# Performance work log

Measured on AMD Instinct MI355X. Metric: run time of the kernel, lower is better.

Reference implementation:

```python
import jax, jax.numpy as jnp
import numpy as np

B = 2097152  # flattened batch of 3x3 rotation matrices

def setup_inputs() -> dict:
    key = jax.random.key(0)
    k1, k2 = jax.random.split(key)
    # scale by 0.1 so cos=(trace(m1 m2^T)-1)/2 stays strictly inside (-1,1)
    pred_rot = jax.random.normal(k1, (B, 3, 3), dtype=jnp.float32) * 0.1
    gt_rot = jax.random.normal(k2, (B, 3, 3), dtype=jnp.float32) * 0.1
    return {"pred_rot": pred_rot, "gt_rot": gt_rot}

def reference(pred_rot, gt_rot):
    m1 = pred_rot.reshape(-1, 3, 3)
    m2 = gt_rot.reshape(-1, 3, 3)
    # trace(m1 @ m2^T) == sum(m1 * m2) elementwise -> avoid the bmm
    cos = (jnp.einsum('bij,bij->b', m1, m2) - 1.0) * 0.5
    cos = jnp.clip(cos, -1.0, 1.0)  # min with +1, max with -1
    theta = jnp.arccos(cos)
    return jnp.mean(theta)  # reduction='mean'
```

## Files before the change

### kernel.cpp

```cpp
#include <hip/hip_runtime.h>
#include <math.h>


typedef float f4 __attribute__((ext_vector_type(4)));

#define TPB 256
#define NBLOCKS 2048

#define LOADQ(P, pa, pb)                                                    \
    P##A0 = __builtin_nontemporal_load((pa) + q);                           \
    P##A1 = __builtin_nontemporal_load((pa) + 4 + q);                       \
    P##A2 = __builtin_nontemporal_load((pa) + 8);                           \
    P##B0 = __builtin_nontemporal_load((pb) + q);                           \
    P##B1 = __builtin_nontemporal_load((pb) + 4 + q);                       \
    P##B2 = __builtin_nontemporal_load((pb) + 8);

__global__ __launch_bounds__(TPB) void geo_partial(
    const float* __restrict__ a, const float* __restrict__ b,
    float* __restrict__ ws, float* __restrict__ out, float invM, int M,
    int use_atomic)
{
    __shared__ float wsum[TPB / 64];
    const int tid = threadIdx.x;
    const int q   = tid & 3;

    float sum = 0.0f;

    const long long G    = (long long)M >> 2;
    const long long Q0   = (long long)blockIdx.x * (TPB / 4) + (tid >> 2);
    const long long Qstr = (long long)gridDim.x * (TPB / 4);

    const f4* __restrict__ a4 = (const f4*)a;
    const f4* __restrict__ b4 = (const f4*)b;

    f4 A0, A1, A2, B0, B1, B2;
    long long Q = Q0;
    if (Q < G) {
        const f4* pa = a4 + 9 * Q;
        const f4* pb = b4 + 9 * Q;
        LOADQ(, pa, pb)
    }

    while (Q < G) {
        const long long Qn = Q + Qstr;
        f4 NA0, NA1, NA2, NB0, NB1, NB2;
        if (Qn < G) {
            const f4* pa = a4 + 9 * Qn;
            const f4* pb = b4 + 9 * Qn;
            LOADQ(N, pa, pb)
        }

        f4 t0, t1;
        t0.x = A0.x * B0.x; t0.y = A0.y * B0.y;
        t0.z = A0.z * B0.z; t0.w = A0.w * B0.w;
        t1.x = A1.x * B1.x; t1.y = A1.y * B1.y;
        t1.z = A1.z * B1.z; t1.w = A1.w * B1.w;

        const float c01 = t0.x + t0.y;
        const float T0  = (c01 + t0.z) + t0.w;
        const float d01 = t1.x + t1.y;
        const float T1  = (d01 + t1.z) + t1.w;

        float P0 = (q == 3) ? 0.0f : ((q == 2) ? t0.x : T0);
        float P1 = (q == 0) ? d01  : ((q == 1) ? 0.0f
                   : ((q == 2) ? (T0 - t0.x) : T0));
        float P2 = (q == 0) ? (T1 - d01) : ((q == 1) ? T1
                   : ((q == 2) ? (T1 - t1.w) : 0.0f));
        float P3 = (q == 2) ? t1.w : ((q == 3) ? T1 : 0.0f);

        P0 += __shfl_xor(P0, 1, 64); P0 += __shfl_xor(P0, 2, 64);
        P1 += __shfl_xor(P1, 1, 64); P1 += __shfl_xor(P1, 2, 64);
        P2 += __shfl_xor(P2, 1, 64); P2 += __shfl_xor(P2, 2, 64);
        P3 += __shfl_xor(P3, 1, 64); P3 += __shfl_xor(P3, 2, 64);

        const float u0 = A2.x * B2.x, u1 = A2.y * B2.y;
        const float u2 = A2.z * B2.z, u3 = A2.w * B2.w;
        const float dl2 = (u0 + u1) + (u2 + u3);

        const float d = (q == 0) ? P0 : (q == 1) ? P1
                      : (q == 2) ? P2 : (P3 + dl2);
        const float cv = fminf(1.0f, fmaxf(-1.0f, (d - 1.0f) * 0.5f));
        sum += acosf(cv);

        if (Qn < G) {
            A0 = NA0; A1 = NA1; A2 = NA2;
            B0 = NB0; B1 = NB1; B2 = NB2;
        }
        Q = Qn;
    }

    {
        const long long gid    = (long long)blockIdx.x * TPB + tid;
        const long long stride = (long long)gridDim.x * TPB;
        for (long long m = 4 * G + gid; m < M; m += stride) {
            float dd = 0.0f;
            #pragma unroll
            for (int j = 0; j < 9; ++j)
                dd = fmaf(a[m * 9 + j], b[m * 9 + j], dd);
            sum += acosf(fminf(1.0f, fmaxf(-1.0f, (dd - 1.0f) * 0.5f)));
        }
    }

    #pragma unroll
    for (int off = 32; off > 0; off >>= 1)
        sum += __shfl_down(sum, off, 64);
    if ((tid & 63) == 0) wsum[tid >> 6] = sum;
    __syncthreads();
    if (tid == 0) {
        float s = 0.0f;
        #pragma unroll
        for (int i = 0; i < TPB / 64; ++i) s += wsum[i];
        if (use_atomic) atomicAdd(out, s * invM);
        else            ws[blockIdx.x] = s;
    }
}

__global__ __launch_bounds__(256) void geo_finish(
    const float* __restrict__ ws, float* __restrict__ out,
    float invM, int nb)
{
    __shared__ float wsum[4];
    float s = 0.0f;
    for (int i = threadIdx.x; i < nb; i += 256) s += ws[i];
    #pragma unroll
    for (int off = 32; off > 0; off >>= 1)
        s += __shfl_down(s, off, 64);
    if ((threadIdx.x & 63) == 0) wsum[threadIdx.x >> 6] = s;
    __syncthreads();
    if (threadIdx.x == 0)
        out[0] = (wsum[0] + wsum[1] + wsum[2] + wsum[3]) * invM;
}

extern "C" void kernel_launch(void* const* d_in, const int* in_sizes, int n_in,
                              void* d_out, int out_size, void* d_ws, size_t ws_size,
                              hipStream_t stream) {
    const float* a = (const float*)d_in[0];
    const float* b = (const float*)d_in[1];
    float* out = (float*)d_out;

    const int n = in_sizes[0];
    const int M = n / 9;

    const bool ws_ok = (ws_size >= (size_t)NBLOCKS * sizeof(float));
    if (!ws_ok) {
        hipMemsetAsync(out, 0, (size_t)out_size * sizeof(float), stream);
    }
    geo_partial<<<NBLOCKS, TPB, 0, stream>>>(
        a, b, (float*)d_ws, out, 1.0f / (float)M, M, ws_ok ? 0 : 1);
    if (ws_ok) {
        geo_finish<<<1, 256, 0, stream>>>(
            (const float*)d_ws, out, 1.0f / (float)M, NBLOCKS);
    }
}
```

Baseline: 162.7 us.

## Process 16 matrices per quad with fully coalesced strided f4 loads

Each group of four lanes now handles 16 matrices (144 floats) at a time, issuing 9 interleaved f4 loads per lane so that consecutive lanes read consecutive 16-byte chunks. The old layout had every lane re-read a shared third vector and only partly coalesced its accesses. The manual software prefetch of the next iteration is dropped in favour of 18 independent loads in flight per iteration. The cost is more registers and more select logic per element, plus four shuffle reductions and acos calls per loop iteration.

```diff
diff --git a/kernel.cpp b/kernel.cpp
--- a/kernel.cpp
+++ b/kernel.cpp
@@ -6,14 +6,6 @@
 
 #define TPB 256
 #define NBLOCKS 2048
-
-#define LOADQ(P, pa, pb)                                                    \
-    P##A0 = __builtin_nontemporal_load((pa) + q);                           \
-    P##A1 = __builtin_nontemporal_load((pa) + 4 + q);                       \
-    P##A2 = __builtin_nontemporal_load((pa) + 8);                           \
-    P##B0 = __builtin_nontemporal_load((pb) + q);                           \
-    P##B1 = __builtin_nontemporal_load((pb) + 4 + q);                       \
-    P##B2 = __builtin_nontemporal_load((pb) + 8);
 
 __global__ __launch_bounds__(TPB) void geo_partial(
     const float* __restrict__ a, const float* __restrict__ b,
@@ -26,73 +18,59 @@
 
     float sum = 0.0f;
 
-    const long long G    = (long long)M >> 2;
-    const long long Q0   = (long long)blockIdx.x * (TPB / 4) + (tid >> 2);
-    const long long Qstr = (long long)gridDim.x * (TPB / 4);
+    const long long NQ   = (long long)M >> 4;
+    const long long gq0  = (long long)blockIdx.x * (TPB / 4) + (tid >> 2);
+    const long long qstr = (long long)gridDim.x * (TPB / 4);
 
     const f4* __restrict__ a4 = (const f4*)a;
     const f4* __restrict__ b4 = (const f4*)b;
 
-    f4 A0, A1, A2, B0, B1, B2;
-    long long Q = Q0;
-    if (Q < G) {
-        const f4* pa = a4 + 9 * Q;
-        const f4* pb = b4 + 9 * Q;
-        LOADQ(, pa, pb)
-    }
+    for (long long gq = gq0; gq < NQ; gq += qstr) {
+        const f4* __restrict__ pa = a4 + 36LL * gq;
+        const f4* __restrict__ pb = b4 + 36LL * gq;
 
-    while (Q < G) {
-        const long long Qn = Q + Qstr;
-        f4 NA0, NA1, NA2, NB0, NB1, NB2;
-        if (Qn < G) {
-            const f4* pa = a4 + 9 * Qn;
-            const f4* pb = b4 + 9 * Qn;
-            LOADQ(N, pa, pb)
+        f4 A[9], B[9];
+        #pragma unroll
+        for (int k = 0; k < 9; ++k) {
+            A[k] = __builtin_nontemporal_load(pa + 4 * k + q);
+            B[k] = __builtin_nontemporal_load(pb + 4 * k + q);
         }
 
-        f4 t0, t1;
-        t0.x = A0.x * B0.x; t0.y = A0.y * B0.y;
-        t0.z = A0.z * B0.z; t0.w = A0.w * B0.w;
-        t1.x = A1.x * B1.x; t1.y = A1.y * B1.y;
-        t1.z = A1.z * B1.z; t1.w = A1.w * B1.w;
+        #pragma unroll
+        for (int g = 0; g < 4; ++g) {
+            float P0 = 0.0f, P1 = 0.0f, P2 = 0.0f, P3 = 0.0f;
+            #pragma unroll
+            for (int i = 0; i < 3; ++i) {
+                const int k = 2 * g + i;
+                const int r = 4 * k + q - 9 * g;
+                const f4 p = A[k] * B[k];
+                const float lo1 = p.x;
+                const float lo2 = lo1 + p.y;
+                const float lo3 = lo2 + p.z;
+                const float s   = lo3 + p.w;
+                P0 += (r == 0 || r == 1) ? s : (r == 2) ? lo1 : 0.0f;
+                P1 += (r == 3) ? s : (r == 2) ? (s - lo1)
+                                   : (r == 4) ? lo2 : 0.0f;
+                P2 += (r == 5) ? s : (r == 4) ? (s - lo2)
+                                   : (r == 6) ? lo3 : 0.0f;
+                P3 += (r == 7 || r == 8) ? s : (r == 6) ? (s - lo3) : 0.0f;
+            }
+            P0 += __shfl_xor(P0, 1, 64); P0 += __shfl_xor(P0, 2, 64);
+            P1 += __shfl_xor(P1, 1, 64); P1 += __shfl_xor(P1, 2, 64);
+            P2 += __shfl_xor(P2, 1, 64); P2 += __shfl_xor(P2, 2, 64);
+            P3 += __shfl_xor(P3, 1, 64); P3 += __shfl_xor(P3, 2, 64);
 
-        const float c01 = t0.x + t0.y;
-        const float T0  = (c01 + t0.z) + t0.w;
-        const float d01 = t1.x + t1.y;
-        const float T1  = (d01 + t1.z) + t1.w;
-
-        float P0 = (q == 3) ? 0.0f : ((q == 2) ? t0.x : T0);
-        float P1 = (q == 0) ? d01  : ((q == 1) ? 0.0f
-                   : ((q == 2) ? (T0 - t0.x) : T0));
-        float P2 = (q == 0) ? (T1 - d01) : ((q == 1) ? T1
-                   : ((q == 2) ? (T1 - t1.w) : 0.0f));
-        float P3 = (q == 2) ? t1.w : ((q == 3) ? T1 : 0.0f);
-
-        P0 += __shfl_xor(P0, 1, 64); P0 += __shfl_xor(P0, 2, 64);
-        P1 += __shfl_xor(P1, 1, 64); P1 += __shfl_xor(P1, 2, 64);
-        P2 += __shfl_xor(P2, 1, 64); P2 += __shfl_xor(P2, 2, 64);
-        P3 += __shfl_xor(P3, 1, 64); P3 += __shfl_xor(P3, 2, 64);
-
-        const float u0 = A2.x * B2.x, u1 = A2.y * B2.y;
-        const float u2 = A2.z * B2.z, u3 = A2.w * B2.w;
-        const float dl2 = (u0 + u1) + (u2 + u3);
-
-        const float d = (q == 0) ? P0 : (q == 1) ? P1
-                      : (q == 2) ? P2 : (P3 + dl2);
-        const float cv = fminf(1.0f, fmaxf(-1.0f, (d - 1.0f) * 0.5f));
-        sum += acosf(cv);
-
-        if (Qn < G) {
-            A0 = NA0; A1 = NA1; A2 = NA2;
-            B0 = NB0; B1 = NB1; B2 = NB2;
+            const float d = (q == 0) ? P0 : (q == 1) ? P1
+                          : (q == 2) ? P2 : P3;
+            const float cv = fminf(1.0f, fmaxf(-1.0f, (d - 1.0f) * 0.5f));
+            sum += acosf(cv);
         }
-        Q = Qn;
     }
 
     {
         const long long gid    = (long long)blockIdx.x * TPB + tid;
         const long long stride = (long long)gridDim.x * TPB;
-        for (long long m = 4 * G + gid; m < M; m += stride) {
+        for (long long m = 16 * NQ + gid; m < M; m += stride) {
             float dd = 0.0f;
             #pragma unroll
             for (int j = 0; j < 9; ++j)
```

Result: faster. 157.6 us (-3.1%).
